# Kernel optimization log

Hardware: AMD Instinct MI355X
Metric: run time of the kernel (lower is better)

## Reference

```python
import jax, jax.numpy as jnp
import numpy as np

B, IC, H, W = 8, 16, 32, 32
OC, KH, KW = 32, 3, 3
PAD, K = 1, 2
OH, OW = H, W  # stride 1, pad 1, dilation 1 with 3x3 kernel
TABLES = OC * IC * KH * KW  # 4608, one LUT per (oc, ic, kh, kw)
M = TABLES * K              # 9216 mask rows
NUM_ENTRIES = 2 ** K


def setup_inputs() -> dict:
    key = jax.random.key(0)
    k1, k2, k3, k4, k5 = jax.random.split(key, 5)
    inp = jax.random.normal(k1, (B, IC, H, W), dtype=jnp.float32)
    w_luts = jax.random.normal(k2, (TABLES, NUM_ENTRIES), dtype=jnp.float32)
    mask_c = jax.random.randint(k3, (M,), 0, IC)
    mask_kh = jax.random.randint(k4, (M,), 0, KH)
    mask_kw = jax.random.randint(k5, (M,), 0, KW)
    return {"input": inp, "w_luts": w_luts, "mask_c": mask_c,
            "mask_kh": mask_kh, "mask_kw": mask_kw}


def _truth_table():
    # tt[j, i] in {-1, +1}: sign of bit j of truth-table entry i
    entries = jnp.arange(NUM_ENTRIES)
    bits = (entries[None, :] >> jnp.arange(K)[:, None]) & 1  # (K, 2^K)
    return (2 * bits - 1).astype(jnp.float32)


def reference(input, w_luts, mask_c, mask_kh, mask_kw):
    # Fused unfold (im2col) + per-table input_mask gather: instead of
    # materializing folded_input (B, L, IC, KH, KW), gather straight from the
    # padded image: expanded[b, oh, ow, m] = padded[b, c_m, oh + kh_m, ow + kw_m]
    padded = jnp.pad(input, ((0, 0), (0, 0), (PAD, PAD), (PAD, PAD)))
    row = jnp.arange(OH)[:, None] + mask_kh[None, :]   # (OH, M)
    col = jnp.arange(OW)[:, None] + mask_kw[None, :]   # (OW, M)
    expanded = padded[:, mask_c[None, None, :], row[:, None, :], col[None, :, :]]  # (B, OH, OW, M)

    # LagrangeTrainer: per-table soft LUT lookup via Lagrange interpolation
    x = expanded.reshape(B * OH * OW, TABLES, K)
    tt = _truth_table()                                       # (K, 2^K)
    factors = (1.0 + x[..., :, None] * tt[None, None]) * 0.5  # (N, T, K, 2^K)
    basis = jnp.prod(factors, axis=-2)                        # (N, T, 2^K)
    out = jnp.einsum('nte,te->nt', basis, w_luts)             # (N, TABLES)

    # Fold-style reshape + sum over the IC*KH*KW tables feeding each output
    out = out.reshape(B, OC, OH, OW, -1).sum(-1)
    out = out.reshape(B, OH * OW, OC).swapaxes(1, 2).reshape(B, OC, OH, OW)
    return out
```

## Files before the change

kernel.cpp:

```cpp
#include <hip/hip_runtime.h>

#define TABLES 4608
#define OC_ 32
#define IC_ 16
#define H_ 32
#define W_ 32
#define B_ 8
#define OH_ 32
#define OW_ 32
#define TPO 144

#define ROWS_PER_WG 8
#define TR 10
#define TC 34
#define CH_STRIDE (TR * TC)
#define TILE_F (IC_ * CH_STRIDE)

struct __align__(16) Rec {
    int   off0;
    int   off1;
    float bb;
    float cc;
    float dd;
    float aa;
    int   pad0, pad1;
};

__global__ __launch_bounds__(256)
void conv_kernel(const float* __restrict__ input,
                 const float* __restrict__ w_luts,
                 const int*   __restrict__ mask_c,
                 const int*   __restrict__ mask_kh,
                 const int*   __restrict__ mask_kw,
                 float*       __restrict__ out) {
    __shared__ float tile[TILE_F];
    __shared__ Rec   srec[TPO];

    const int oh0 = blockIdx.x * ROWS_PER_WG;
    const int oc  = blockIdx.y;
    const int b   = blockIdx.z;
    const int tid = threadIdx.x;

    const float* inb = input + b * (IC_ * H_ * W_);
    for (int u = tid; u < IC_ * TR * 8; u += 256) {
        int ch  = u / 80;
        int rem = u - ch * 80;
        int r   = rem >> 3;
        int c4  = (rem & 7) * 4;
        int grow = oh0 + r - 1;
        float4 v = make_float4(0.f, 0.f, 0.f, 0.f);
        if ((unsigned)grow < (unsigned)H_)
            v = *reinterpret_cast<const float4*>(inb + (ch * H_ + grow) * W_ + c4);
        float* dst = &tile[ch * CH_STRIDE + r * TC + 1 + c4];
        dst[0] = v.x; dst[1] = v.y; dst[2] = v.z; dst[3] = v.w;
    }
    for (int i = tid; i < IC_ * TR * 2; i += 256) {
        int ch  = i / 20;
        int rem = i - ch * 20;
        int r   = rem >> 1;
        int cc  = (rem & 1) ? (TC - 1) : 0;
        tile[ch * CH_STRIDE + r * TC + cc] = 0.f;
    }
    if (tid < TPO) {
        int t  = oc * TPO + tid;
        const float4 w = *reinterpret_cast<const float4*>(w_luts + 4 * t);
        int m0 = 2 * t, m1 = m0 + 1;
        Rec r;
        r.off0 = mask_c[m0] * CH_STRIDE + mask_kh[m0] * TC + mask_kw[m0];
        r.off1 = mask_c[m1] * CH_STRIDE + mask_kh[m1] * TC + mask_kw[m1];
        r.aa = 0.25f * ( w.x + w.y + w.z + w.w);
        r.bb = 0.25f * (-w.x + w.y - w.z + w.w);
        r.cc = 0.25f * (-w.x - w.y + w.z + w.w);
        r.dd = 0.25f * ( w.x - w.y - w.z + w.w);
        r.pad0 = 0; r.pad1 = 0;
        srec[tid] = r;
    }
    __syncthreads();

    const int lo   = tid >> 5;
    const int ow   = tid & 31;
    const int base = lo * TC + ow;
    const int oh   = oh0 + lo;

    float acc = 0.0f;
    #pragma unroll 8
    for (int t = 0; t < TPO; ++t) {
        Rec r = srec[t];
        float x0 = tile[base + r.off0];
        float x1 = tile[base + r.off1];
        acc += r.aa;
        acc = fmaf(r.bb, x0, acc);
        acc = fmaf(x1, fmaf(r.dd, x0, r.cc), acc);
    }
    out[((b * OC_ + oc) * OH_ + oh) * OW_ + ow] = acc;
}

extern "C" void kernel_launch(void* const* d_in, const int* in_sizes, int n_in,
                              void* d_out, int out_size, void* d_ws, size_t ws_size,
                              hipStream_t stream) {
    const float* input   = (const float*)d_in[0];
    const float* w_luts  = (const float*)d_in[1];
    const int*   mask_c  = (const int*)d_in[2];
    const int*   mask_kh = (const int*)d_in[3];
    const int*   mask_kw = (const int*)d_in[4];
    float* out = (float*)d_out;

    conv_kernel<<<dim3(OH_ / ROWS_PER_WG, OC_, B_), dim3(256), 0, stream>>>(
        input, w_luts, mask_c, mask_kh, mask_kw, out);
}
```

Baseline: 77.97 us.

## Compute two output rows per thread and pack LUT records into 16 bytes

Each workgroup now covers 16 output rows, and each thread accumulates two rows 8 apart, so every LUT record read from shared memory is reused across two outputs. The record shrinks to 16 bytes: the two byte offsets are packed into one int, and the constant term is summed once per block as a bias instead of being added every iteration. The larger tile (18 rows) raises LDS use and halves the grid to 512 workgroups, which may lower occupancy and latency hiding. The record setup is moved ahead of the tile load.

Result: faster. 72.73 us (-6.7%).

```diff
diff --git a/kernel.cpp b/kernel.cpp
--- a/kernel.cpp
+++ b/kernel.cpp
@@ -1,30 +1,19 @@
 #include <hip/hip_runtime.h>
 
-#define TABLES 4608
 #define OC_ 32
 #define IC_ 16
 #define H_ 32
 #define W_ 32
 #define B_ 8
-#define OH_ 32
-#define OW_ 32
 #define TPO 144
 
-#define ROWS_PER_WG 8
-#define TR 10
+#define ROWS_PER_WG 16
+#define TR 18
 #define TC 34
 #define CH_STRIDE (TR * TC)
 #define TILE_F (IC_ * CH_STRIDE)
 
-struct __align__(16) Rec {
-    int   off0;
-    int   off1;
-    float bb;
-    float cc;
-    float dd;
-    float aa;
-    int   pad0, pad1;
-};
+struct alignas(16) Rec4 { int offs; float bb, cc, dd; };
 
 __global__ __launch_bounds__(256)
 void conv_kernel(const float* __restrict__ input,
@@ -34,17 +23,34 @@
                  const int*   __restrict__ mask_kw,
                  float*       __restrict__ out) {
     __shared__ float tile[TILE_F];
-    __shared__ Rec   srec[TPO];
+    __shared__ Rec4  srec[TPO];
+    __shared__ float sAA[TPO];
+    __shared__ float sP[8];
 
     const int oh0 = blockIdx.x * ROWS_PER_WG;
     const int oc  = blockIdx.y;
     const int b   = blockIdx.z;
     const int tid = threadIdx.x;
 
+    if (tid < TPO) {
+        int t = oc * TPO + tid;
+        const float4 w = *reinterpret_cast<const float4*>(w_luts + 4 * t);
+        int m0 = 2 * t, m1 = m0 + 1;
+        int off0 = mask_c[m0] * CH_STRIDE + mask_kh[m0] * TC + mask_kw[m0];
+        int off1 = mask_c[m1] * CH_STRIDE + mask_kh[m1] * TC + mask_kw[m1];
+        Rec4 r;
+        r.offs = (off0 * 4) | ((off1 * 4) << 16);
+        r.bb = 0.25f * (-w.x + w.y - w.z + w.w);
+        r.cc = 0.25f * (-w.x - w.y + w.z + w.w);
+        r.dd = 0.25f * ( w.x - w.y - w.z + w.w);
+        srec[tid] = r;
+        sAA[tid]  = 0.25f * (w.x + w.y + w.z + w.w);
+    }
+
     const float* inb = input + b * (IC_ * H_ * W_);
     for (int u = tid; u < IC_ * TR * 8; u += 256) {
-        int ch  = u / 80;
-        int rem = u - ch * 80;
+        int ch  = u / (TR * 8);
+        int rem = u - ch * (TR * 8);
         int r   = rem >> 3;
         int c4  = (rem & 7) * 4;
         int grow = oh0 + r - 1;
@@ -55,44 +61,52 @@
         dst[0] = v.x; dst[1] = v.y; dst[2] = v.z; dst[3] = v.w;
     }
     for (int i = tid; i < IC_ * TR * 2; i += 256) {
-        int ch  = i / 20;
-        int rem = i - ch * 20;
+        int ch  = i / (TR * 2);
+        int rem = i - ch * (TR * 2);
         int r   = rem >> 1;
-        int cc  = (rem & 1) ? (TC - 1) : 0;
-        tile[ch * CH_STRIDE + r * TC + cc] = 0.f;
-    }
-    if (tid < TPO) {
-        int t  = oc * TPO + tid;
-        const float4 w = *reinterpret_cast<const float4*>(w_luts + 4 * t);
-        int m0 = 2 * t, m1 = m0 + 1;
-        Rec r;
-        r.off0 = mask_c[m0] * CH_STRIDE + mask_kh[m0] * TC + mask_kw[m0];
-        r.off1 = mask_c[m1] * CH_STRIDE + mask_kh[m1] * TC + mask_kw[m1];
-        r.aa = 0.25f * ( w.x + w.y + w.z + w.w);
-        r.bb = 0.25f * (-w.x + w.y - w.z + w.w);
-        r.cc = 0.25f * (-w.x - w.y + w.z + w.w);
-        r.dd = 0.25f * ( w.x - w.y - w.z + w.w);
-        r.pad0 = 0; r.pad1 = 0;
-        srec[tid] = r;
+        int cc2 = (rem & 1) ? (TC - 1) : 0;
+        tile[ch * CH_STRIDE + r * TC + cc2] = 0.f;
     }
     __syncthreads();
 
-    const int lo   = tid >> 5;
-    const int ow   = tid & 31;
-    const int base = lo * TC + ow;
-    const int oh   = oh0 + lo;
+    if (tid < 8) {
+        float s = 0.f;
+        #pragma unroll
+        for (int i = 0; i < 18; ++i) s += sAA[tid * 18 + i];
+        sP[tid] = s;
+    }
+    __syncthreads();
+    const float bias = ((sP[0] + sP[1]) + (sP[2] + sP[3]))
+                     + ((sP[4] + sP[5]) + (sP[6] + sP[7]));
 
-    float acc = 0.0f;
+    const int rl    = tid >> 5;
+    const int ow    = tid & 31;
+    const int baseA = (rl * TC + ow) * 4;
+    const int baseB = baseA + 8 * TC * 4;
+    const char* tbase = (const char*)tile;
+
+    float accA = 0.f, accB = 0.f;
     #pragma unroll 8
     for (int t = 0; t < TPO; ++t) {
-        Rec r = srec[t];
-        float x0 = tile[base + r.off0];
-        float x1 = tile[base + r.off1];
-        acc += r.aa;
-        acc = fmaf(r.bb, x0, acc);
-        acc = fmaf(x1, fmaf(r.dd, x0, r.cc), acc);
+        const int4 q = *reinterpret_cast<const int4*>(&srec[t]);
+        const int   offs = q.x;
+        const float bb = __int_as_float(q.y);
+        const float cc = __int_as_float(q.z);
+        const float dd = __int_as_float(q.w);
+        const int o0 = offs & 0xffff;
+        const int o1 = ((unsigned)offs) >> 16;
+        float x0a = *reinterpret_cast<const float*>(tbase + baseA + o0);
+        float x1a = *reinterpret_cast<const float*>(tbase + baseA + o1);
+        float x0b = *reinterpret_cast<const float*>(tbase + baseB + o0);
+        float x1b = *reinterpret_cast<const float*>(tbase + baseB + o1);
+        accA = fmaf(bb, x0a, accA);
+        accA = fmaf(x1a, fmaf(dd, x0a, cc), accA);
+        accB = fmaf(bb, x0b, accB);
+        accB = fmaf(x1b, fmaf(dd, x0b, cc), accB);
     }
-    out[((b * OC_ + oc) * OH_ + oh) * OW_ + ow] = acc;
+    const int ohA = oh0 + rl;
+    out[((b * OC_ + oc) * H_ + ohA    ) * W_ + ow] = accA + bias;
+    out[((b * OC_ + oc) * H_ + ohA + 8) * W_ + ow] = accB + bias;
 }
 
 extern "C" void kernel_launch(void* const* d_in, const int* in_sizes, int n_in,
@@ -105,6 +119,6 @@
     const int*   mask_kw = (const int*)d_in[4];
     float* out = (float*)d_out;
 
-    conv_kernel<<<dim3(OH_ / ROWS_PER_WG, OC_, B_), dim3(256), 0, stream>>>(
+    conv_kernel<<<dim3(H_ / ROWS_PER_WG, OC_, B_), dim3(256), 0, stream>>>(
         input, w_luts, mask_c, mask_kh, mask_kw, out);
 }
```
